# Performance work log

Hardware: AMD Instinct MI355X
Metric: run time of the kernel (lower is better)

## Reference

```python
import jax, jax.numpy as jnp
import numpy as np

INPUT_H = 512
INPUT_W = 512
POOL = 5
BN_EPS = 1e-5


def setup_inputs() -> dict:
    key = jax.random.key(0)
    ks = jax.random.split(key, 8)
    B = 16
    c3 = jax.random.normal(ks[0], (B, 512, 64, 64), jnp.float32)
    c4 = jax.random.normal(ks[1], (B, 1024, 32, 32), jnp.float32)
    xy = jax.random.uniform(ks[2], (B, 10, 4), jnp.float32) * 512.0
    # ensure x1<=x2, y1<=y2 like real detector boxes
    boxes = jnp.concatenate([jnp.minimum(xy[..., :2], xy[..., 2:]),
                             jnp.maximum(xy[..., :2], xy[..., 2:])], axis=-1)
    w_conv = jax.random.normal(ks[3], (512, 1536), jnp.float32) * 0.02  # 1x1 conv kernel
    b_conv = jnp.zeros((512,), jnp.float32)
    bn_gamma = jnp.ones((512,), jnp.float32)
    bn_beta = jnp.zeros((512,), jnp.float32)
    bn_mean = jax.random.normal(ks[4], (512,), jnp.float32) * 0.1
    bn_var = jax.random.uniform(ks[5], (512,), jnp.float32) * 0.5 + 0.5
    return {"c3": c3, "c4": c4, "boxes": boxes, "w_conv": w_conv, "b_conv": b_conv,
            "bn_gamma": bn_gamma, "bn_beta": bn_beta, "bn_mean": bn_mean, "bn_var": bn_var}


def _bin_weights(lo, hi, size, nout):
    """Adaptive-avg-pool bin weights over axis of length `size` for crop [lo,hi).
    Returns [nout, size] row-stochastic matrix (same math as AdaptiveAvgPool1d bins)."""
    length = hi - lo
    k = jnp.arange(nout)
    starts = lo + (k * length) // nout                      # floor(k*L/n)
    ends = lo + ((k + 1) * length + nout - 1) // nout        # ceil((k+1)*L/n)
    idx = jnp.arange(size)
    mask = (idx[None, :] >= starts[:, None]) & (idx[None, :] < ends[:, None])
    return mask.astype(jnp.float32) / (ends - starts)[:, None].astype(jnp.float32)


def reference(c3, c4, boxes, w_conv, b_conv, bn_gamma, bn_beta, bn_mean, bn_var):
    B = c3.shape[0]
    c4u = jax.image.resize(c4, (B, c4.shape[1], c4.shape[2] * 2, c4.shape[3] * 2),
                           method='bilinear')
    fused = jnp.concatenate([c3, c4u], axis=1)               # [B,1536,H,W]
    y = jnp.einsum('bchw,oc->bohw', fused, w_conv) + b_conv[None, :, None, None]
    inv = bn_gamma / jnp.sqrt(bn_var + BN_EPS)               # eval-mode BN
    y = y * inv[None, :, None, None] + (bn_beta - bn_mean * inv)[None, :, None, None]
    attr_blob = jax.nn.relu(y)                               # [B,512,H,W]
    H, W = attr_blob.shape[-2:]
    sx = W / INPUT_W
    sy = H / INPUT_H

    def pool_one(feat, box):  # feat [C,H,W], box [4] -> [C,5,5]
        x1 = jnp.clip(jnp.floor(box[0] * sx), 0, W - 1).astype(jnp.int32)
        y1 = jnp.clip(jnp.floor(box[1] * sy), 0, H - 1).astype(jnp.int32)
        x2 = jnp.clip(jnp.ceil(box[2] * sx), 0, W - 1).astype(jnp.int32)
        y2 = jnp.clip(jnp.ceil(box[3] * sy), 0, H - 1).astype(jnp.int32)
        x2 = jnp.where(x2 <= x1, jnp.minimum(x1 + 1, W), x2)
        y2 = jnp.where(y2 <= y1, jnp.minimum(y1 + 1, H), y2)
        wy = _bin_weights(y1, y2, H, POOL)                   # [5,H]
        wx = _bin_weights(x1, x2, W, POOL)                   # [5,W]
        return jnp.einsum('ph,chw,qw->cpq', wy, feat, wx)

    obj_blob = jax.vmap(lambda f, bx: jax.vmap(lambda b: pool_one(f, b))(bx))(attr_blob, boxes)
    return boxes, obj_blob  # ([B,10,4], [B,10,512,5,5])
```

## Files before the change

kernel.cpp:

```cpp
#include <hip/hip_runtime.h>
#include <stdint.h>

#define FH 64
#define FW 64
#define CIN 1536
#define C3C 512
#define C4C 1024
#define COUT 512
#define BATCH 16
#define NPIX 4096
#define NBOX 10
#define MPAD 256
#define KT128 12

typedef float v4f __attribute__((ext_vector_type(4)));

#define GLOAD_LDS16(g, l) __builtin_amdgcn_global_load_lds( \
    (const __attribute__((address_space(1))) void*)(g),     \
    (__attribute__((address_space(3))) void*)(l), 16, 0, 0)

#define BARRIER() asm volatile("s_barrier" ::: "memory")

__device__ __forceinline__ uint32_t pack4_fp8(float a, float b, float c, float d) {
    int lo = __builtin_amdgcn_cvt_pk_fp8_f32(a, b, 0, false);
    int v  = __builtin_amdgcn_cvt_pk_fp8_f32(c, d, lo, true);
    return (uint32_t)v;
}
__device__ __forceinline__ unsigned char f32_to_fp8(float a) {
    return (unsigned char)(__builtin_amdgcn_cvt_pk_fp8_f32(a, a, 0, false) & 0xff);
}

__global__ void prep_bn(const float* __restrict__ bng, const float* __restrict__ bnb,
                        const float* __restrict__ bnm, const float* __restrict__ bnv,
                        const float* __restrict__ bconv,
                        float* __restrict__ scale, float* __restrict__ shift) {
    int o = threadIdx.x;
    if (o < COUT) {
        float inv = bng[o] / sqrtf(bnv[o] + 1e-5f);
        scale[o] = inv * 0.0625f;
        shift[o] = bnb[o] + inv * (bconv[o] - bnm[o]);
    }
}

__global__ void conv_w(const float* __restrict__ w, uint32_t* __restrict__ w8, int n4) {
    int i = blockIdx.x * 256 + threadIdx.x;
    if (i < n4) {
        float4 f = *(const float4*)(w + i * 4);
        w8[i] = pack4_fp8(f.x * 16.0f, f.y * 16.0f, f.z * 16.0f, f.w * 16.0f);
    }
}

__global__ __launch_bounds__(256) void build_fusedT(const float* __restrict__ c3,
                                                    const float* __restrict__ c4,
                                                    unsigned char* __restrict__ fusedT) {
    __shared__ uint32_t lds[64 * 36];
    int ct = blockIdx.x;
    int y  = blockIdx.y;
    int b  = blockIdx.z;
    int t  = threadIdx.x;
    int pg = t & 15;
    int cq = t >> 4;

    #pragma unroll
    for (int r = 0; r < 2; ++r) {
        int cquad = cq + 16 * r;
        float vv[4][4];
        if (ct < 4) {
            int ch = ct * 128 + 4 * cquad;
            const float* src = c3 + (((size_t)(b * C3C + ch) * FH + y) * FW) + 4 * pg;
            #pragma unroll
            for (int k = 0; k < 4; ++k) {
                float4 f = *(const float4*)(src + (size_t)k * (FH * FW));
                vv[k][0] = f.x; vv[k][1] = f.y; vv[k][2] = f.z; vv[k][3] = f.w;
            }
        } else {
            int ch = ct * 128 - 512 + 4 * cquad;
            int jy = y >> 1;
            int jyB = min(max(jy + ((y & 1) ? 1 : -1), 0), 31);
            const float* base = c4 + (size_t)(b * C4C + ch) * 1024;
            #pragma unroll
            for (int k = 0; k < 4; ++k) {
                const float* pc = base + (size_t)k * 1024;
                float2 f0 = *(const float2*)(pc + jy * 32 + 2 * pg);
                float2 f1 = *(const float2*)(pc + jyB * 32 + 2 * pg);
                float rbA = 0.75f * f0.x + 0.25f * f1.x;
                float rbB = 0.75f * f0.y + 0.25f * f1.y;
                float rbm = __shfl_up(rbB, 1, 16);
                float rbp = __shfl_down(rbA, 1, 16);
                if (pg == 0)  rbm = rbA;
                if (pg == 15) rbp = rbB;
                vv[k][0] = 0.75f * rbA + 0.25f * rbm;
                vv[k][1] = 0.75f * rbA + 0.25f * rbB;
                vv[k][2] = 0.75f * rbB + 0.25f * rbA;
                vv[k][3] = 0.75f * rbB + 0.25f * rbp;
            }
        }
        #pragma unroll
        for (int i = 0; i < 4; ++i) {
            int px = 4 * pg + i;
            lds[px * 36 + 4 * ((cquad >> 2) ^ ((px >> 1) & 7)) + (cquad & 3)] =
                pack4_fp8(vv[0][i], vv[1][i], vv[2][i], vv[3][i]);
        }
    }
    __syncthreads();
    int g = t & 7;
    #pragma unroll
    for (int rr = 0; rr < 2; ++rr) {
        int px = (t >> 3) + 32 * rr;
        uint4 w = *(const uint4*)(&lds[px * 36 + 4 * (g ^ ((px >> 1) & 7))]);
        *(uint4*)(fusedT + ((size_t)b * NPIX + y * FW + px) * CIN + ct * 128 + g * 16) = w;
    }
}

__global__ __launch_bounds__(512, 2) void gemm_bn_relu(
        const unsigned char* __restrict__ w8,
        const unsigned char* __restrict__ fusedT,
        const float* __restrict__ scale, const float* __restrict__ shift,
        unsigned char* __restrict__ attr) {
    __shared__ __align__(16) unsigned char lds_a[2][32768];
    __shared__ __align__(16) unsigned char lds_b[2][32768];
    const int t  = threadIdx.x;
    const int n0 = blockIdx.x * 256;
    const int o0 = blockIdx.y * 256;
    const int b  = blockIdx.z;
    const int wave = t >> 6, lane = t & 63;
    const int wm = wave & 1, wn = wave >> 1;
    const int quad = lane >> 4, l16 = lane & 15;
    const int q2 = quad >> 1, q1 = (quad & 1) * 8;
    int cs[4];
    #pragma unroll
    for (int s = 0; s < 4; ++s) cs[s] = (((2 * s + q2) ^ (l16 & 7)) * 16) + q1;
    const unsigned char* fb = fusedT + (size_t)b * NPIX * CIN;

    const int rr = t >> 3;
    const int cg = (t & 7) ^ (rr & 7);
    const unsigned char* gA = w8 + (size_t)(o0 + rr) * CIN + cg * 16;
    const unsigned char* gB = fb + (size_t)(n0 + rr) * CIN + cg * 16;

#define SA(u, kt, d) GLOAD_LDS16(gA + (size_t)(u) * (64 * CIN) + (kt) * 128, \
                                 &lds_a[d][(u) * 8192 + t * 16])
#define SB(u, kt, d) GLOAD_LDS16(gB + (size_t)(u) * (64 * CIN) + (kt) * 128, \
                                 &lds_b[d][(u) * 8192 + t * 16])
#define RA(d, ph, i, s) (*(const long*)(&lds_a[d][((wm * 128 + (ph) * 64 + (i) * 16 + l16) << 7) + cs[s]]))
#define RB(d, j, s)     (*(const long*)(&lds_b[d][((wn * 64 + (j) * 16 + l16) << 7) + cs[s]]))

    v4f acc[8][4];
    #pragma unroll
    for (int i = 0; i < 8; ++i)
        #pragma unroll
        for (int j = 0; j < 4; ++j) acc[i][j] = (v4f)0.0f;

    SA(0, 0, 0); SA(1, 0, 0); SA(2, 0, 0); SA(3, 0, 0);
    SB(0, 0, 0); SB(1, 0, 0); SB(2, 0, 0); SB(3, 0, 0);
    SA(0, 1, 1); SA(2, 1, 1); SB(0, 1, 1); SB(1, 1, 1); SB(2, 1, 1); SB(3, 1, 1);
    asm volatile("s_waitcnt vmcnt(6)" ::: "memory");
    BARRIER();

    long af[4][4], bf[4][4];

    for (int kt = 0; kt < KT128; ++kt) {
        const int cur = kt & 1, nxt = cur ^ 1;

        #pragma unroll
        for (int i = 0; i < 4; ++i)
            #pragma unroll
            for (int s = 0; s < 4; ++s) af[i][s] = RA(cur, 0, i, s);
        #pragma unroll
        for (int j = 0; j < 4; ++j)
            #pragma unroll
            for (int s = 0; s < 4; ++s) bf[j][s] = RB(cur, j, s);
        if (kt > 0 && kt + 1 < KT128) {
            SA(0, kt + 1, nxt); SA(2, kt + 1, nxt);
            SB(0, kt + 1, nxt); SB(1, kt + 1, nxt);
            SB(2, kt + 1, nxt); SB(3, kt + 1, nxt);
        }
        BARRIER();
        __builtin_amdgcn_s_setprio(1);
        #pragma unroll
        for (int s = 0; s < 4; ++s)
            #pragma unroll
            for (int i = 0; i < 4; ++i)
                #pragma unroll
                for (int j = 0; j < 4; ++j)
                    acc[i][j] = __builtin_amdgcn_mfma_f32_16x16x32_fp8_fp8(af[i][s], bf[j][s], acc[i][j], 0, 0, 0);
        __builtin_amdgcn_s_setprio(0);
        if (kt + 1 < KT128) { asm volatile("s_waitcnt vmcnt(6)" ::: "memory"); }
        else               { asm volatile("s_waitcnt vmcnt(0)" ::: "memory"); }
        BARRIER();

        #pragma unroll
        for (int i = 0; i < 4; ++i)
            #pragma unroll
            for (int s = 0; s < 4; ++s) af[i][s] = RA(cur, 1, i, s);
        if (kt + 1 < KT128) { SA(1, kt + 1, nxt); SA(3, kt + 1, nxt); }
        BARRIER();
        __builtin_amdgcn_s_setprio(1);
        #pragma unroll
        for (int s = 0; s < 4; ++s)
            #pragma unroll
            for (int i = 0; i < 4; ++i)
                #pragma unroll
                for (int j = 0; j < 4; ++j)
                    acc[4 + i][j] = __builtin_amdgcn_mfma_f32_16x16x32_fp8_fp8(af[i][s], bf[j][s], acc[4 + i][j], 0, 0, 0);
        __builtin_amdgcn_s_setprio(0);
        if (kt + 1 < KT128) { asm volatile("s_waitcnt vmcnt(2)" ::: "memory"); }
        BARRIER();
    }

    unsigned char* ab = attr + (size_t)b * COUT * NPIX;
    #pragma unroll
    for (int a = 0; a < 8; ++a) {
        int obase = o0 + wm * 128 + (a >> 2) * 64 + (a & 3) * 16 + quad * 4;
        #pragma unroll
        for (int r = 0; r < 4; ++r) {
            int oo = obase + r;
            float sc = scale[oo], sh = shift[oo];
            #pragma unroll
            for (int j = 0; j < 4; ++j) {
                int n = n0 + wn * 64 + j * 16 + l16;
                float v = fmaxf(acc[a][j][r] * sc + sh, 0.0f);
                ab[(size_t)oo * NPIX + n] = f32_to_fp8(v);
            }
        }
    }
#undef SA
#undef SB
#undef RA
#undef RB
}

__global__ __launch_bounds__(256) void build_P(const float* __restrict__ boxes,
                                               unsigned char* __restrict__ P) {
    int br  = blockIdx.x;
    int m25 = blockIdx.y;
    int b   = br / NBOX;
    int m   = (br % NBOX) * 25 + m25;
    int p   = m25 / 5, q = m25 % 5;
    int t   = threadIdx.x;
    int y   = t >> 2;
    int x0  = (t & 3) * 16;
    const float* bx = boxes + (size_t)br * 4;
    int x1 = min(max((int)floorf(bx[0] * 0.125f), 0), 63);
    int y1 = min(max((int)floorf(bx[1] * 0.125f), 0), 63);
    int x2 = min(max((int)ceilf (bx[2] * 0.125f), 0), 63);
    int y2 = min(max((int)ceilf (bx[3] * 0.125f), 0), 63);
    if (x2 <= x1) x2 = min(x1 + 1, 64);
    if (y2 <= y1) y2 = min(y1 + 1, 64);
    int Lx = x2 - x1, Ly = y2 - y1;
    int sx = x1 + (q * Lx) / 5;
    int ex = x1 + ((q + 1) * Lx + 4) / 5;
    int sy = y1 + (p * Ly) / 5;
    int ey = y1 + ((p + 1) * Ly + 4) / 5;
    float wyv  = (y >= sy && y < ey) ? 1.0f / (float)(ey - sy) : 0.0f;
    float pval = 64.0f * wyv / (float)(ex - sx);
    float v[16];
    #pragma unroll
    for (int i = 0; i < 16; ++i) {
        int xi = x0 + i;
        v[i] = (xi >= sx && xi < ex) ? pval : 0.0f;
    }
    uint4 w;
    w.x = pack4_fp8(v[0],  v[1],  v[2],  v[3]);
    w.y = pack4_fp8(v[4],  v[5],  v[6],  v[7]);
    w.z = pack4_fp8(v[8],  v[9],  v[10], v[11]);
    w.w = pack4_fp8(v[12], v[13], v[14], v[15]);
    *(uint4*)(P + ((size_t)b * MPAD + m) * NPIX + y * FW + x0) = w;
}

__global__ __launch_bounds__(256) void pool_gemm(
        const unsigned char* __restrict__ P,
        const unsigned char* __restrict__ attr,
        float* __restrict__ part2) {
    __shared__ __align__(16) unsigned char lds_a[128 * 64];
    __shared__ __align__(16) unsigned char lds_b[128 * 64];
    int t  = threadIdx.x;
    int m0 = blockIdx.x * 128;
    int c0 = (blockIdx.y & 3) * 128;
    int seg = blockIdx.y >> 2;
    int b  = blockIdx.z;
    int wave = t >> 6, lane = t & 63;
    int wm = wave & 1, wn = wave >> 1;
    int quad = lane >> 4, l16 = lane & 15;
    const unsigned char* Pb = P + (size_t)b * MPAD * NPIX + seg * 1024;
    const unsigned char* ab = attr + (size_t)b * COUT * NPIX + seg * 1024;

    v4f acc[4][4];
    #pragma unroll
    for (int i = 0; i < 4; ++i)
        #pragma unroll
        for (int j = 0; j < 4; ++j) acc[i][j] = (v4f)0.0f;

    int row = t >> 2;
    int cg  = (t & 3) ^ ((row >> 1) & 3);
    const unsigned char* ga0 = Pb + (size_t)(m0 + row) * NPIX + cg * 16;
    const unsigned char* ga1 = Pb + (size_t)(m0 + row + 64) * NPIX + cg * 16;
    const unsigned char* gb0 = ab + (size_t)(c0 + row) * NPIX + cg * 16;
    const unsigned char* gb1 = ab + (size_t)(c0 + row + 64) * NPIX + cg * 16;
    unsigned char* la0 = lds_a + t * 16;
    unsigned char* la1 = lds_a + 4096 + t * 16;
    unsigned char* lb0 = lds_b + t * 16;
    unsigned char* lb1 = lds_b + 4096 + t * 16;

    int ra[4], rb[4];
    #pragma unroll
    for (int i = 0; i < 4; ++i) { ra[i] = wm * 64 + i * 16 + l16; rb[i] = wn * 64 + i * 16 + l16; }
    int q2 = quad >> 1, q1 = (quad & 1) * 8;

    for (int kt = 0; kt < 1024 / 64; ++kt) {
        __syncthreads();
        GLOAD_LDS16(ga0, la0);
        GLOAD_LDS16(ga1, la1);
        GLOAD_LDS16(gb0, lb0);
        GLOAD_LDS16(gb1, lb1);
        ga0 += 64; ga1 += 64; gb0 += 64; gb1 += 64;
        __syncthreads();

        #pragma unroll
        for (int s = 0; s < 2; ++s) {
            long af[4], bf[4];
            #pragma unroll
            for (int i = 0; i < 4; ++i) {
                int pa = (2 * s + q2) ^ ((ra[i] >> 1) & 3);
                af[i] = *(const long*)(lds_a + ra[i] * 64 + pa * 16 + q1);
                int pb = (2 * s + q2) ^ ((rb[i] >> 1) & 3);
                bf[i] = *(const long*)(lds_b + rb[i] * 64 + pb * 16 + q1);
            }
            #pragma unroll
            for (int i = 0; i < 4; ++i)
                #pragma unroll
                for (int j = 0; j < 4; ++j)
                    acc[i][j] = __builtin_amdgcn_mfma_f32_16x16x32_fp8_fp8(af[i], bf[j], acc[i][j], 0, 0, 0);
        }
    }

    float* pp = part2 + (((size_t)seg * BATCH + b) * MPAD) * COUT;
    #pragma unroll
    for (int i = 0; i < 4; ++i) {
        #pragma unroll
        for (int r = 0; r < 4; ++r) {
            int mrow = m0 + wm * 64 + i * 16 + quad * 4 + r;
            #pragma unroll
            for (int j = 0; j < 4; ++j) {
                int c = c0 + wn * 64 + j * 16 + l16;
                pp[(size_t)mrow * COUT + c] = acc[i][j][r];
            }
        }
    }
}

__global__ __launch_bounds__(256) void pool_reduce(const float* __restrict__ part2,
                                                   float* __restrict__ out) {
    const size_t SEG = (size_t)BATCH * MPAD * COUT;
    int i = blockIdx.x * 256 + threadIdx.x;
    int c = i & (COUT - 1);
    int m = (i >> 9) & (MPAD - 1);
    int b = i >> 17;
    if (m >= 250) return;
    float s = part2[i] + part2[i + SEG] + part2[i + 2 * SEG] + part2[i + 3 * SEG];
    int box = m / 25, bin = m - box * 25;
    out[640 + ((size_t)(b * NBOX + box) * COUT + c) * 25 + bin] = s * 0.015625f;
}

extern "C" void kernel_launch(void* const* d_in, const int* in_sizes, int n_in,
                              void* d_out, int out_size, void* d_ws, size_t ws_size,
                              hipStream_t stream) {
    const float* c3     = (const float*)d_in[0];
    const float* c4     = (const float*)d_in[1];
    const float* boxes  = (const float*)d_in[2];
    const float* w_conv = (const float*)d_in[3];
    const float* b_conv = (const float*)d_in[4];
    const float* bng    = (const float*)d_in[5];
    const float* bnb    = (const float*)d_in[6];
    const float* bnm    = (const float*)d_in[7];
    const float* bnv    = (const float*)d_in[8];
    float* out = (float*)d_out;

    char* ws = (char*)d_ws;
    unsigned char* fusedT = (unsigned char*)ws;
    unsigned char* P      = (unsigned char*)(ws + 100663296);
    float*         part2  = (float*)(ws + 117440512);
    unsigned char* w8     = (unsigned char*)(ws + 150994944);
    float*         scale  = (float*)(ws + 151781376);
    float*         shift  = (float*)(ws + 151783424);
    unsigned char* attr   = (unsigned char*)(ws + 151785472);

    hipMemcpyAsync(d_out, d_in[2], 640 * sizeof(float), hipMemcpyDeviceToDevice, stream);
    prep_bn<<<1, 512, 0, stream>>>(bng, bnb, bnm, bnv, b_conv, scale, shift);
    conv_w<<<(COUT * CIN / 4 + 255) / 256, 256, 0, stream>>>(w_conv, (uint32_t*)w8, COUT * CIN / 4);
    build_P<<<dim3(160, 25), 256, 0, stream>>>(boxes, P);
    build_fusedT<<<dim3(12, 64, 16), 256, 0, stream>>>(c3, c4, fusedT);
    gemm_bn_relu<<<dim3(16, 2, 16), 512, 0, stream>>>(w8, fusedT, scale, shift, attr);
    pool_gemm<<<dim3(2, 16, 16), 256, 0, stream>>>(P, attr, part2);
    pool_reduce<<<(BATCH * MPAD * COUT) / 256, 256, 0, stream>>>(part2, out);
    (void)in_sizes; (void)n_in; (void)out_size; (void)ws_size;
}
```

Measured before the change: 415.5 us.

## Permute K within 128-chunks so GEMM fragments load as 16-byte LDS reads

The weight and activation producers now write each 128-element K chunk in a permuted order. In that order the 8-byte MFMA operands for different k-steps sit next to each other, so the GEMM can fetch two operands with one 16-byte LDS read instead of two 8-byte reads. The change also drops the barrier between the fragment loads and the MFMA blocks in both phases. Because both operands are permuted the same way along K, the reduction result is unchanged. Fewer, wider LDS instructions cut issue overhead. Removing the barriers risks ordering hazards if the later waitcnt and barrier structure does not fully cover them, and the producers now do narrower 8-byte global stores.

```diff
diff --git a/kernel.cpp b/kernel.cpp
--- a/kernel.cpp
+++ b/kernel.cpp
@@ -14,6 +14,7 @@
 #define KT128 12
 
 typedef float v4f __attribute__((ext_vector_type(4)));
+typedef long  v2l __attribute__((ext_vector_type(2)));
 
 #define GLOAD_LDS16(g, l) __builtin_amdgcn_global_load_lds( \
     (const __attribute__((address_space(1))) void*)(g),     \
@@ -29,6 +30,7 @@
 __device__ __forceinline__ unsigned char f32_to_fp8(float a) {
     return (unsigned char)(__builtin_amdgcn_cvt_pk_fp8_f32(a, a, 0, false) & 0xff);
 }
+
 
 __global__ void prep_bn(const float* __restrict__ bng, const float* __restrict__ bnb,
                         const float* __restrict__ bnm, const float* __restrict__ bnv,
@@ -42,11 +44,16 @@
     }
 }
 
-__global__ void conv_w(const float* __restrict__ w, uint32_t* __restrict__ w8, int n4) {
+__global__ void conv_w(const float* __restrict__ w, unsigned char* __restrict__ w8, int n4) {
     int i = blockIdx.x * 256 + threadIdx.x;
     if (i < n4) {
         float4 f = *(const float4*)(w + i * 4);
-        w8[i] = pack4_fp8(f.x * 16.0f, f.y * 16.0f, f.z * 16.0f, f.w * 16.0f);
+        uint32_t v = pack4_fp8(f.x * 16.0f, f.y * 16.0f, f.z * 16.0f, f.w * 16.0f);
+        int c0 = (i * 4) % CIN;
+        int o  = (i * 4) / CIN;
+        int k7 = c0 & 127;
+        int pos = ((k7 >> 3) & 3) * 32 + (k7 >> 5) * 8 + (k7 & 7);
+        *(uint32_t*)(w8 + (size_t)o * CIN + (c0 & ~127) + pos) = v;
     }
 }
 
@@ -105,10 +112,14 @@
     __syncthreads();
     int g = t & 7;
     #pragma unroll
-    for (int rr = 0; rr < 2; ++rr) {
-        int px = (t >> 3) + 32 * rr;
+    for (int rr2 = 0; rr2 < 2; ++rr2) {
+        int px = (t >> 3) + 32 * rr2;
         uint4 w = *(const uint4*)(&lds[px * 36 + 4 * (g ^ ((px >> 1) & 7))]);
-        *(uint4*)(fusedT + ((size_t)b * NPIX + y * FW + px) * CIN + ct * 128 + g * 16) = w;
+        unsigned char* dst = fusedT + ((size_t)b * NPIX + y * FW + px) * CIN + ct * 128;
+        int pos0 = ((2 * g) & 3) * 32 + (g >> 1) * 8;
+        int pos1 = ((2 * g + 1) & 3) * 32 + (g >> 1) * 8;
+        *(uint2*)(dst + pos0) = make_uint2(w.x, w.y);
+        *(uint2*)(dst + pos1) = make_uint2(w.z, w.w);
     }
 }
 
@@ -126,10 +137,8 @@
     const int wave = t >> 6, lane = t & 63;
     const int wm = wave & 1, wn = wave >> 1;
     const int quad = lane >> 4, l16 = lane & 15;
-    const int q2 = quad >> 1, q1 = (quad & 1) * 8;
-    int cs[4];
-    #pragma unroll
-    for (int s = 0; s < 4; ++s) cs[s] = (((2 * s + q2) ^ (l16 & 7)) * 16) + q1;
+    const int cp0 = (((quad << 1) ^ (l16 & 7)) << 4);
+    const int cp1 = cp0 ^ 16;
     const unsigned char* fb = fusedT + (size_t)b * NPIX * CIN;
 
     const int rr = t >> 3;
@@ -141,8 +150,8 @@
                                  &lds_a[d][(u) * 8192 + t * 16])
 #define SB(u, kt, d) GLOAD_LDS16(gB + (size_t)(u) * (64 * CIN) + (kt) * 128, \
                                  &lds_b[d][(u) * 8192 + t * 16])
-#define RA(d, ph, i, s) (*(const long*)(&lds_a[d][((wm * 128 + (ph) * 64 + (i) * 16 + l16) << 7) + cs[s]]))
-#define RB(d, j, s)     (*(const long*)(&lds_b[d][((wn * 64 + (j) * 16 + l16) << 7) + cs[s]]))
+#define RAV(d, ph, i, cp) (*(const v2l*)(&lds_a[d][((wm * 128 + (ph) * 64 + (i) * 16 + l16) << 7) + (cp)]))
+#define RBV(d, j, cp)     (*(const v2l*)(&lds_b[d][((wn * 64 + (j) * 16 + l16) << 7) + (cp)]))
 
     v4f acc[8][4];
     #pragma unroll
@@ -156,52 +165,58 @@
     asm volatile("s_waitcnt vmcnt(6)" ::: "memory");
     BARRIER();
 
-    long af[4][4], bf[4][4];
+    v2l ah0[4], ah1[4], bh0[4], bh1[4];
 
     for (int kt = 0; kt < KT128; ++kt) {
         const int cur = kt & 1, nxt = cur ^ 1;
 
         #pragma unroll
-        for (int i = 0; i < 4; ++i)
-            #pragma unroll
-            for (int s = 0; s < 4; ++s) af[i][s] = RA(cur, 0, i, s);
-        #pragma unroll
-        for (int j = 0; j < 4; ++j)
-            #pragma unroll
-            for (int s = 0; s < 4; ++s) bf[j][s] = RB(cur, j, s);
+        for (int i = 0; i < 4; ++i) { ah0[i] = RAV(cur, 0, i, cp0); ah1[i] = RAV(cur, 0, i, cp1); }
+        #pragma unroll
+        for (int j = 0; j < 4; ++j) { bh0[j] = RBV(cur, j, cp0); bh1[j] = RBV(cur, j, cp1); }
         if (kt > 0 && kt + 1 < KT128) {
             SA(0, kt + 1, nxt); SA(2, kt + 1, nxt);
             SB(0, kt + 1, nxt); SB(1, kt + 1, nxt);
             SB(2, kt + 1, nxt); SB(3, kt + 1, nxt);
         }
-        BARRIER();
         __builtin_amdgcn_s_setprio(1);
         #pragma unroll
-        for (int s = 0; s < 4; ++s)
+        for (int s = 0; s < 2; ++s)
             #pragma unroll
             for (int i = 0; i < 4; ++i)
                 #pragma unroll
                 for (int j = 0; j < 4; ++j)
-                    acc[i][j] = __builtin_amdgcn_mfma_f32_16x16x32_fp8_fp8(af[i][s], bf[j][s], acc[i][j], 0, 0, 0);
+                    acc[i][j] = __builtin_amdgcn_mfma_f32_16x16x32_fp8_fp8(ah0[i][s], bh0[j][s], acc[i][j], 0, 0, 0);
+        #pragma unroll
+        for (int s = 0; s < 2; ++s)
+            #pragma unroll
+            for (int i = 0; i < 4; ++i)
+                #pragma unroll
+                for (int j = 0; j < 4; ++j)
+                    acc[i][j] = __builtin_amdgcn_mfma_f32_16x16x32_fp8_fp8(ah1[i][s], bh1[j][s], acc[i][j], 0, 0, 0);
         __builtin_amdgcn_s_setprio(0);
         if (kt + 1 < KT128) { asm volatile("s_waitcnt vmcnt(6)" ::: "memory"); }
         else               { asm volatile("s_waitcnt vmcnt(0)" ::: "memory"); }
         BARRIER();
 
         #pragma unroll
-        for (int i = 0; i < 4; ++i)
-            #pragma unroll
-            for (int s = 0; s < 4; ++s) af[i][s] = RA(cur, 1, i, s);
+        for (int i = 0; i < 4; ++i) { ah0[i] = RAV(cur, 1, i, cp0); ah1[i] = RAV(cur, 1, i, cp1); }
         if (kt + 1 < KT128) { SA(1, kt + 1, nxt); SA(3, kt + 1, nxt); }
-        BARRIER();
         __builtin_amdgcn_s_setprio(1);
         #pragma unroll
-        for (int s = 0; s < 4; ++s)
+        for (int s = 0; s < 2; ++s)
             #pragma unroll
             for (int i = 0; i < 4; ++i)
                 #pragma unroll
                 for (int j = 0; j < 4; ++j)
-                    acc[4 + i][j] = __builtin_amdgcn_mfma_f32_16x16x32_fp8_fp8(af[i][s], bf[j][s], acc[4 + i][j], 0, 0, 0);
+                    acc[4 + i][j] = __builtin_amdgcn_mfma_f32_16x16x32_fp8_fp8(ah0[i][s], bh0[j][s], acc[4 + i][j], 0, 0, 0);
+        #pragma unroll
+        for (int s = 0; s < 2; ++s)
+            #pragma unroll
+            for (int i = 0; i < 4; ++i)
+                #pragma unroll
+                for (int j = 0; j < 4; ++j)
+                    acc[4 + i][j] = __builtin_amdgcn_mfma_f32_16x16x32_fp8_fp8(ah1[i][s], bh1[j][s], acc[4 + i][j], 0, 0, 0);
         __builtin_amdgcn_s_setprio(0);
         if (kt + 1 < KT128) { asm volatile("s_waitcnt vmcnt(2)" ::: "memory"); }
         BARRIER();
@@ -225,8 +240,8 @@
     }
 #undef SA
 #undef SB
-#undef RA
-#undef RB
+#undef RAV
+#undef RBV
 }
 
 __global__ __launch_bounds__(256) void build_P(const float* __restrict__ boxes,
@@ -386,7 +401,7 @@
 
     hipMemcpyAsync(d_out, d_in[2], 640 * sizeof(float), hipMemcpyDeviceToDevice, stream);
     prep_bn<<<1, 512, 0, stream>>>(bng, bnb, bnm, bnv, b_conv, scale, shift);
-    conv_w<<<(COUT * CIN / 4 + 255) / 256, 256, 0, stream>>>(w_conv, (uint32_t*)w8, COUT * CIN / 4);
+    conv_w<<<(COUT * CIN / 4 + 255) / 256, 256, 0, stream>>>(w_conv, w8, COUT * CIN / 4);
     build_P<<<dim3(160, 25), 256, 0, stream>>>(boxes, P);
     build_fusedT<<<dim3(12, 64, 16), 256, 0, stream>>>(c3, c4, fusedT);
     gemm_bn_relu<<<dim3(16, 2, 16), 512, 0, stream>>>(w8, fusedT, scale, shift, attr);
```

Measured after the change: 395.0 us. 1.05x faster.
